# Kernel tuning notes

Measured on AMD Instinct MI355X. Metric: run time of the kernel, lower is better.

## Reference

```python
import jax, jax.numpy as jnp
import numpy as np

T, B, D_IN, NQ = 256, 2048, 128, 8  # time, batch, input_dim, n_qubits == hidden_dim


def setup_inputs() -> dict:
    key = jax.random.key(0)
    ks = jax.random.split(key, 13)
    s = 1.0 / np.sqrt(D_IN + NQ)
    def lin(ka, kb):
        W = jax.random.uniform(ka, (D_IN + NQ, NQ), jnp.float32, -s, s)
        b = jax.random.uniform(kb, (NQ,), jnp.float32, -s, s)
        return W, b
    Wf, bf = lin(ks[0], ks[1])
    Wi, bi = lin(ks[2], ks[3])
    Wg, bg = lin(ks[4], ks[5])
    Wo, bo = lin(ks[6], ks[7])
    # trainable RX angles per wire for each of the 4 quantum gates
    thf = jax.random.normal(ks[8], (NQ,), jnp.float32) * 0.1
    thi = jax.random.normal(ks[9], (NQ,), jnp.float32) * 0.1
    thg = jax.random.normal(ks[10], (NQ,), jnp.float32) * 0.1
    tho = jax.random.normal(ks[11], (NQ,), jnp.float32) * 0.1
    inputs = jax.random.normal(ks[12], (T, B, D_IN), jnp.float32)
    return {"inputs": inputs, "Wf": Wf, "bf": bf, "Wi": Wi, "bi": bi,
            "Wg": Wg, "bg": bg, "Wo": Wo, "bo": bo,
            "thf": thf, "thi": thi, "thg": thg, "tho": tho}


def _qgate(lin_out, theta):
    # |0..0> -> RX(x_i) encode -> RX(theta_i) trainable -> <PauliZ_i> = cos(x_i + theta_i)
    return jnp.cos(lin_out + theta)


def reference(inputs, Wf, bf, Wi, bi, Wg, bg, Wo, bo, thf, thi, thg, tho):
    Bsz = inputs.shape[1]
    h0 = jnp.zeros((Bsz, NQ), inputs.dtype)
    c0 = jnp.zeros((Bsz, NQ), inputs.dtype)

    def step(carry, x):
        hx, cx = carry
        comb = jnp.concatenate([x, hx], axis=1)  # [B, D_IN+NQ]
        f = jax.nn.sigmoid(_qgate(comb @ Wf + bf, thf))
        i = jax.nn.sigmoid(_qgate(comb @ Wi + bi, thi))
        g = jnp.tanh(_qgate(comb @ Wg + bg, thg))
        o = jax.nn.sigmoid(_qgate(comb @ Wo + bo, tho))
        cx = f * cx + i * g
        hx = o * jnp.tanh(cx)
        return (hx, cx), hx

    (hx, cx), outputs = jax.lax.scan(step, (h0, c0), inputs)
    return outputs, hx, cx
```

## Files before the change

### kernel.cpp

```cpp
#include <hip/hip_runtime.h>

#define T_DIM 256
#define B_DIM 2048
#define D_IN_DIM 128
#define NQ 8
#define ROWS_PER_BLK 64
#define XSTRIDE 129

__global__ __launch_bounds__(256) void qlstm_gemm(
    const float* __restrict__ X,
    const float* __restrict__ Wf, const float* __restrict__ Wi,
    const float* __restrict__ Wg, const float* __restrict__ Wo,
    const float* __restrict__ bf, const float* __restrict__ bi,
    const float* __restrict__ bg, const float* __restrict__ bo,
    const float* __restrict__ thf, const float* __restrict__ thi,
    const float* __restrict__ thg, const float* __restrict__ tho,
    float* __restrict__ Z, int plane_stride)
{
    __shared__ float xs[ROWS_PER_BLK * XSTRIDE];

    const int t = (int)threadIdx.x;
    const int r0 = (int)blockIdx.x * ROWS_PER_BLK;

    const float4* Xg = (const float4*)(X + (size_t)r0 * D_IN_DIM);
#pragma unroll
    for (int i = 0; i < 8; i++) {
        int L = t + i * 256;
        float4 v = Xg[L];
        int row = L >> 5;
        int k4  = L & 31;
        float* d = &xs[row * XSTRIDE + k4 * 4];
        d[0] = v.x; d[1] = v.y; d[2] = v.z; d[3] = v.w;
    }
    __syncthreads();

    const int wid  = __builtin_amdgcn_readfirstlane(t >> 6);
    const int lane = t & 63;

    const float* W  = (wid == 0) ? Wf  : (wid == 1) ? Wi  : (wid == 2) ? Wg  : Wo;
    const float* BB = (wid == 0) ? bf  : (wid == 1) ? bi  : (wid == 2) ? bg  : bo;
    const float* TH = (wid == 0) ? thf : (wid == 1) ? thi : (wid == 2) ? thg : tho;

    float acc[NQ];
#pragma unroll
    for (int q = 0; q < NQ; q++) acc[q] = BB[q] + TH[q];

    const float* xrow = &xs[lane * XSTRIDE];
#pragma unroll 4
    for (int k = 0; k < D_IN_DIM; k++) {
        float xk = xrow[k];
#pragma unroll
        for (int q = 0; q < NQ; q++)
            acc[q] += xk * W[k * NQ + q];
    }

    float* Zg = Z + (size_t)wid * plane_stride + (size_t)(r0 + lane) * NQ;
    ((float4*)Zg)[0] = make_float4(acc[0], acc[1], acc[2], acc[3]);
    ((float4*)Zg)[1] = make_float4(acc[4], acc[5], acc[6], acc[7]);
}

__device__ __forceinline__ float fast_sig(float x)  { return 1.0f / (1.0f + __expf(-x)); }
__device__ __forceinline__ float fast_tanh(float x) { return 1.0f - 2.0f / (__expf(2.0f * x) + 1.0f); }

__global__ __launch_bounds__(64) void qlstm_recur(
    const float* __restrict__ Z,
    const float* __restrict__ Wf, const float* __restrict__ Wi,
    const float* __restrict__ Wg, const float* __restrict__ Wo,
    float* __restrict__ out,
    float* __restrict__ state,
    int t0, int ct, int plane_stride, int first, int last)
{
    const int tid  = (int)blockIdx.x * 64 + (int)threadIdx.x;
    const int b    = tid >> 3;
    const int q    = tid & 7;
    const int base = ((int)threadIdx.x) & ~7;

    float whf[8], whi[8], whg[8], who[8];
#pragma unroll
    for (int j = 0; j < 8; j++) {
        whf[j] = Wf[(D_IN_DIM + j) * NQ + q];
        whi[j] = Wi[(D_IN_DIM + j) * NQ + q];
        whg[j] = Wg[(D_IN_DIM + j) * NQ + q];
        who[j] = Wo[(D_IN_DIM + j) * NQ + q];
    }

    float h, c;
    if (first) { h = 0.0f; c = 0.0f; }
    else       { h = state[tid]; c = state[B_DIM * NQ + tid]; }

    const float* Zp = Z + tid;
    const size_t ps = (size_t)plane_stride;
    const size_t stepsz = (size_t)B_DIM * NQ;

    float cf0 = Zp[0], ci0 = Zp[ps], cg0 = Zp[2 * ps], co0 = Zp[3 * ps];
    size_t o1 = (ct > 1) ? stepsz : 0;
    float cf1 = Zp[o1], ci1 = Zp[ps + o1], cg1 = Zp[2 * ps + o1], co1 = Zp[3 * ps + o1];

    for (int tl = 0; tl < ct; tl++) {
        int tn = (tl + 2 < ct) ? (tl + 2) : (ct - 1);
        size_t on = (size_t)tn * stepsz;
        float nf = Zp[on], ni = Zp[ps + on], ng = Zp[2 * ps + on], no = Zp[3 * ps + on];

        float accf = cf0, acci = ci0, accg = cg0, acco = co0;
#pragma unroll
        for (int j = 0; j < 8; j++) {
            float hj = __shfl(h, base + j, 64);
            accf += hj * whf[j];
            acci += hj * whi[j];
            accg += hj * whg[j];
            acco += hj * who[j];
        }

        float fg = fast_sig(__cosf(accf));
        float ig = fast_sig(__cosf(acci));
        float gg = fast_tanh(__cosf(accg));
        float og = fast_sig(__cosf(acco));

        c = fg * c + ig * gg;
        h = og * fast_tanh(c);

        out[(size_t)(t0 + tl) * stepsz + tid] = h;

        cf0 = cf1; ci0 = ci1; cg0 = cg1; co0 = co1;
        cf1 = nf;  ci1 = ni;  cg1 = ng;  co1 = no;
    }

    if (last) {
        out[(size_t)T_DIM * stepsz + tid] = h;
        out[(size_t)T_DIM * stepsz + stepsz + tid] = c;
    } else {
        state[tid] = h;
        state[B_DIM * NQ + tid] = c;
    }
}

extern "C" void kernel_launch(void* const* d_in, const int* in_sizes, int n_in,
                              void* d_out, int out_size, void* d_ws, size_t ws_size,
                              hipStream_t stream) {
    const float* X   = (const float*)d_in[0];
    const float* Wf  = (const float*)d_in[1];
    const float* bf  = (const float*)d_in[2];
    const float* Wi  = (const float*)d_in[3];
    const float* bi  = (const float*)d_in[4];
    const float* Wg  = (const float*)d_in[5];
    const float* bg  = (const float*)d_in[6];
    const float* Wo  = (const float*)d_in[7];
    const float* bo  = (const float*)d_in[8];
    const float* thf = (const float*)d_in[9];
    const float* thi = (const float*)d_in[10];
    const float* thg = (const float*)d_in[11];
    const float* tho = (const float*)d_in[12];
    float* out = (float*)d_out;

    const size_t state_bytes = (size_t)2 * B_DIM * NQ * sizeof(float);
    float* state = (float*)d_ws;
    float* Zbuf  = (float*)((char*)d_ws + state_bytes);
    size_t avail = ws_size > state_bytes ? ws_size - state_bytes : 0;
    const size_t z_bytes_per_t = (size_t)B_DIM * 32 * sizeof(float);
    int maxChunkT = (int)(avail / z_bytes_per_t);
    if (maxChunkT > T_DIM) maxChunkT = T_DIM;
    if (maxChunkT < 1) maxChunkT = 1;

    int t0 = 0;
    int first = 1;
    while (t0 < T_DIM) {
        int ct = (T_DIM - t0 < maxChunkT) ? (T_DIM - t0) : maxChunkT;
        int rows = ct * B_DIM;
        int plane_stride = rows * NQ;
        qlstm_gemm<<<rows / ROWS_PER_BLK, 256, 0, stream>>>(
            X + (size_t)t0 * B_DIM * D_IN_DIM,
            Wf, Wi, Wg, Wo, bf, bi, bg, bo, thf, thi, thg, tho,
            Zbuf, plane_stride);
        int last = (t0 + ct == T_DIM) ? 1 : 0;
        qlstm_recur<<<(B_DIM * NQ) / 64, 64, 0, stream>>>(
            Zbuf, Wf, Wi, Wg, Wo, out, state, t0, ct, plane_stride, first, last);
        t0 += ct;
        first = 0;
    }
}
```

Baseline: 501.8 us.

## Interleave gate preactivations as float4, deepen prefetch, use ds_swizzle broadcast

The GEMM kernel now transposes its results through shared memory so that the four gate preactivations for each (row, qubit) are stored together as one float4. The recurrent kernel then loads a single float4 per step instead of four scattered floats. It also keeps an 8-step register prefetch ring to hide global latency in the serial loop, and replaces __shfl with ds_swizzle broadcasts within each group of 8 lanes. The chunk size is rounded down to a multiple of 8, which assumes ct is at least 8 and a multiple of 8. The GEMM kernel gains extra syncs and an LDS round-trip.

```diff
diff --git a/kernel.cpp b/kernel.cpp
--- a/kernel.cpp
+++ b/kernel.cpp
@@ -6,6 +6,7 @@
 #define NQ 8
 #define ROWS_PER_BLK 64
 #define XSTRIDE 129
+#define TSTRIDE 33
 
 __global__ __launch_bounds__(256) void qlstm_gemm(
     const float* __restrict__ X,
@@ -15,7 +16,7 @@
     const float* __restrict__ bg, const float* __restrict__ bo,
     const float* __restrict__ thf, const float* __restrict__ thi,
     const float* __restrict__ thg, const float* __restrict__ tho,
-    float* __restrict__ Z, int plane_stride)
+    float4* __restrict__ Z)
 {
     __shared__ float xs[ROWS_PER_BLK * XSTRIDE];
 
@@ -54,26 +55,56 @@
             acc[q] += xk * W[k * NQ + q];
     }
 
-    float* Zg = Z + (size_t)wid * plane_stride + (size_t)(r0 + lane) * NQ;
-    ((float4*)Zg)[0] = make_float4(acc[0], acc[1], acc[2], acc[3]);
-    ((float4*)Zg)[1] = make_float4(acc[4], acc[5], acc[6], acc[7]);
+    __syncthreads();
+    float* tile = xs;
+#pragma unroll
+    for (int q = 0; q < NQ; q++)
+        tile[lane * TSTRIDE + q * 4 + wid] = acc[q];
+    __syncthreads();
+
+    float4* Zblk = Z + (size_t)r0 * NQ;
+#pragma unroll
+    for (int i = 0; i < 2; i++) {
+        int F = t + i * 256;
+        int r = F >> 3, q = F & 7;
+        const float* s = &tile[r * TSTRIDE + q * 4];
+        Zblk[F] = make_float4(s[0], s[1], s[2], s[3]);
+    }
 }
 
 __device__ __forceinline__ float fast_sig(float x)  { return 1.0f / (1.0f + __expf(-x)); }
 __device__ __forceinline__ float fast_tanh(float x) { return 1.0f - 2.0f / (__expf(2.0f * x) + 1.0f); }
 
+#define BCAST8(x, J) \
+    __int_as_float(__builtin_amdgcn_ds_swizzle(__float_as_int(x), ((J) << 5) | 0x18))
+
+#define DOT_TERM(J) { \
+    float hj = BCAST8(h, J); \
+    accf += hj * whf[J]; acci += hj * whi[J]; \
+    accg += hj * whg[J]; acco += hj * who[J]; }
+
+#define LSTM_STEP(zv, outp) { \
+    float accf = (zv).x, acci = (zv).y, accg = (zv).z, acco = (zv).w; \
+    DOT_TERM(0) DOT_TERM(1) DOT_TERM(2) DOT_TERM(3) \
+    DOT_TERM(4) DOT_TERM(5) DOT_TERM(6) DOT_TERM(7) \
+    float fg = fast_sig(__cosf(accf)); \
+    float ig = fast_sig(__cosf(acci)); \
+    float gg = fast_tanh(__cosf(accg)); \
+    float og = fast_sig(__cosf(acco)); \
+    c = fg * c + ig * gg; \
+    h = og * fast_tanh(c); \
+    *(outp) = h; }
+
 __global__ __launch_bounds__(64) void qlstm_recur(
-    const float* __restrict__ Z,
+    const float4* __restrict__ Z,
     const float* __restrict__ Wf, const float* __restrict__ Wi,
     const float* __restrict__ Wg, const float* __restrict__ Wo,
     float* __restrict__ out,
     float* __restrict__ state,
-    int t0, int ct, int plane_stride, int first, int last)
+    int t0, int ct, int first, int last)
 {
-    const int tid  = (int)blockIdx.x * 64 + (int)threadIdx.x;
-    const int b    = tid >> 3;
-    const int q    = tid & 7;
-    const int base = ((int)threadIdx.x) & ~7;
+    const int tid = (int)blockIdx.x * 64 + (int)threadIdx.x;
+    const int q   = tid & 7;
 
     float whf[8], whi[8], whg[8], who[8];
 #pragma unroll
@@ -88,41 +119,30 @@
     if (first) { h = 0.0f; c = 0.0f; }
     else       { h = state[tid]; c = state[B_DIM * NQ + tid]; }
 
-    const float* Zp = Z + tid;
-    const size_t ps = (size_t)plane_stride;
     const size_t stepsz = (size_t)B_DIM * NQ;
-
-    float cf0 = Zp[0], ci0 = Zp[ps], cg0 = Zp[2 * ps], co0 = Zp[3 * ps];
-    size_t o1 = (ct > 1) ? stepsz : 0;
-    float cf1 = Zp[o1], ci1 = Zp[ps + o1], cg1 = Zp[2 * ps + o1], co1 = Zp[3 * ps + o1];
-
-    for (int tl = 0; tl < ct; tl++) {
-        int tn = (tl + 2 < ct) ? (tl + 2) : (ct - 1);
-        size_t on = (size_t)tn * stepsz;
-        float nf = Zp[on], ni = Zp[ps + on], ng = Zp[2 * ps + on], no = Zp[3 * ps + on];
-
-        float accf = cf0, acci = ci0, accg = cg0, acco = co0;
-#pragma unroll
-        for (int j = 0; j < 8; j++) {
-            float hj = __shfl(h, base + j, 64);
-            accf += hj * whf[j];
-            acci += hj * whi[j];
-            accg += hj * whg[j];
-            acco += hj * who[j];
+    const float4* Zp = Z + tid;
+    float* outp = out + (size_t)t0 * stepsz + tid;
+
+    float4 buf[8];
+#pragma unroll
+    for (int s = 0; s < 8; s++) buf[s] = Zp[(size_t)s * stepsz];
+
+    int tb = 0;
+    for (; tb + 8 < ct; tb += 8) {
+#pragma unroll
+        for (int s = 0; s < 8; s++) {
+            float4 nz = Zp[(size_t)(tb + s + 8) * stepsz];
+            float4 z = buf[s];
+            LSTM_STEP(z, outp)
+            outp += stepsz;
+            buf[s] = nz;
         }
-
-        float fg = fast_sig(__cosf(accf));
-        float ig = fast_sig(__cosf(acci));
-        float gg = fast_tanh(__cosf(accg));
-        float og = fast_sig(__cosf(acco));
-
-        c = fg * c + ig * gg;
-        h = og * fast_tanh(c);
-
-        out[(size_t)(t0 + tl) * stepsz + tid] = h;
-
-        cf0 = cf1; ci0 = ci1; cg0 = cg1; co0 = co1;
-        cf1 = nf;  ci1 = ni;  cg1 = ng;  co1 = no;
+    }
+#pragma unroll
+    for (int s = 0; s < 8; s++) {
+        float4 z = buf[s];
+        LSTM_STEP(z, outp)
+        outp += stepsz;
     }
 
     if (last) {
@@ -154,26 +174,26 @@
 
     const size_t state_bytes = (size_t)2 * B_DIM * NQ * sizeof(float);
     float* state = (float*)d_ws;
-    float* Zbuf  = (float*)((char*)d_ws + state_bytes);
+    float4* Zbuf = (float4*)((char*)d_ws + state_bytes);
     size_t avail = ws_size > state_bytes ? ws_size - state_bytes : 0;
-    const size_t z_bytes_per_t = (size_t)B_DIM * 32 * sizeof(float);
+    const size_t z_bytes_per_t = (size_t)B_DIM * NQ * sizeof(float4);
     int maxChunkT = (int)(avail / z_bytes_per_t);
     if (maxChunkT > T_DIM) maxChunkT = T_DIM;
-    if (maxChunkT < 1) maxChunkT = 1;
+    maxChunkT &= ~7;
+    if (maxChunkT < 8) maxChunkT = 8;
 
     int t0 = 0;
     int first = 1;
     while (t0 < T_DIM) {
         int ct = (T_DIM - t0 < maxChunkT) ? (T_DIM - t0) : maxChunkT;
         int rows = ct * B_DIM;
-        int plane_stride = rows * NQ;
         qlstm_gemm<<<rows / ROWS_PER_BLK, 256, 0, stream>>>(
             X + (size_t)t0 * B_DIM * D_IN_DIM,
             Wf, Wi, Wg, Wo, bf, bi, bg, bo, thf, thi, thg, tho,
-            Zbuf, plane_stride);
+            Zbuf);
         int last = (t0 + ct == T_DIM) ? 1 : 0;
         qlstm_recur<<<(B_DIM * NQ) / 64, 64, 0, stream>>>(
-            Zbuf, Wf, Wi, Wg, Wo, out, state, t0, ct, plane_stride, first, last);
+            Zbuf, Wf, Wi, Wg, Wo, out, state, t0, ct, first, last);
         t0 += ct;
         first = 0;
     }
```

Measured after the change: 496.5 us. Within noise of the previous version (-1.0%).
